# Optimization experiments

Hardware: AMD Instinct MI355X
Metric: run time of the kernel (lower is better)

The kernel has to match this reference:

```python
import jax, jax.numpy as jnp
import numpy as np

B, S, D, H = 2, 2048, 1024, 16
DK = D // H  # 64


def setup_inputs() -> dict:
    key = jax.random.key(0)
    ks = jax.random.split(key, 9)
    scale = 1.0 / np.sqrt(D)
    inp = {
        "q": jax.random.normal(ks[0], (B, S, D), dtype=jnp.float32),
        "k": jax.random.normal(ks[1], (B, S, D), dtype=jnp.float32),
        "v": jax.random.normal(ks[2], (B, S, D), dtype=jnp.float32),
        "Wq": jax.random.normal(ks[3], (D, D), dtype=jnp.float32) * scale,
        "bq": jax.random.normal(ks[4], (D,), dtype=jnp.float32) * scale,
        "Wk": jax.random.normal(ks[5], (D, D), dtype=jnp.float32) * scale,
        "bk": jax.random.normal(ks[6], (D,), dtype=jnp.float32) * scale,
        "Wv": jax.random.normal(ks[7], (D, D), dtype=jnp.float32) * scale,
        "bv": jax.random.normal(ks[8], (D,), dtype=jnp.float32) * scale,
        "mask": jnp.tril(jnp.ones((S, S), dtype=jnp.int32))[None, None],  # [1,1,S,S] causal
    }
    return inp


def reference(q, k, v, Wq, bq, Wk, bk, Wv, bv, mask):
    b, s, d = q.shape
    # QKV projections -> [B, H, S, DK]
    qh = (q @ Wq + bq).reshape(b, s, H, DK).transpose(0, 2, 1, 3)
    kh = (k @ Wk + bk).reshape(b, s, H, DK).transpose(0, 2, 1, 3)
    vh = (v @ Wv + bv).reshape(b, s, H, DK).transpose(0, 2, 1, 3)
    # scores [B, H, Sq, Sk]
    scores = jnp.einsum("bhqd,bhkd->bhqk", qh, kh) / jnp.sqrt(jnp.float32(DK))
    scores = jnp.where(mask == 0, jnp.float32(-1e9), scores)
    attn = jax.nn.softmax(scores, axis=-1)  # dropout is identity at inference
    out = jnp.einsum("bhqk,bhkd->bhqd", attn, vh)
    return out.transpose(0, 2, 1, 3).reshape(b, s, d)
```

## Files before the change

### kernel.cpp

```cpp
#include <hip/hip_runtime.h>
#include <hip/hip_bf16.h>

#define D_MODEL 1024
#define SEQ 2048
#define NH 16
#define DKH 64
#define MROWS 4096

typedef __attribute__((ext_vector_type(8))) short bf16x8;
typedef __attribute__((ext_vector_type(4))) float f32x4;
typedef __attribute__((ext_vector_type(4))) int int4v;

__device__ inline short f2bf(float f) {
    __hip_bfloat16 h = __float2bfloat16(f);
    return __builtin_bit_cast(short, h);
}

#define GLOAD16(gsrc, ldst)                                                     \
    __builtin_amdgcn_global_load_lds(                                           \
        (const __attribute__((address_space(1))) void*)(gsrc),                  \
        (__attribute__((address_space(3))) void*)(ldst), 16, 0, 0)

__global__ __launch_bounds__(256) void prep_kernel(
    const float* __restrict__ q, const float* __restrict__ k,
    const float* __restrict__ v,
    const float* __restrict__ Wq, const float* __restrict__ Wk,
    const float* __restrict__ Wv,
    short* __restrict__ aqkv, short* __restrict__ Wt) {
    __shared__ float tile[32][33];
    const int bx = blockIdx.x;
    if (bx < 6144) {
        const int z = bx >> 11;
        const int blk = bx & 2047;
        const float* src = (z == 0) ? q : (z == 1) ? k : v;
        short* dst = aqkv + (size_t)z * MROWS * D_MODEL;
        const size_t i = ((size_t)blk * 256 + threadIdx.x) * 8;
        float4 f0 = *(const float4*)(src + i);
        float4 f1 = *(const float4*)(src + i + 4);
        bf16x8 p;
        p[0] = f2bf(f0.x); p[1] = f2bf(f0.y); p[2] = f2bf(f0.z); p[3] = f2bf(f0.w);
        p[4] = f2bf(f1.x); p[5] = f2bf(f1.y); p[6] = f2bf(f1.z); p[7] = f2bf(f1.w);
        *(bf16x8*)(dst + i) = p;
    } else {
        int b = bx - 6144;
        const int z = b >> 10; b &= 1023;
        const float* W = (z == 0) ? Wq : (z == 1) ? Wk : Wv;
        short* dst = Wt + (size_t)z * D_MODEL * D_MODEL;
        const int n0 = (b & 31) * 32, k0 = (b >> 5) * 32;
        const int tx = threadIdx.x & 31, ty = threadIdx.x >> 5;
        for (int i = 0; i < 4; ++i)
            tile[ty + 8 * i][tx] = W[(size_t)(k0 + ty + 8 * i) * D_MODEL + n0 + tx];
        __syncthreads();
        for (int i = 0; i < 4; ++i)
            dst[(size_t)(n0 + ty + 8 * i) * D_MODEL + k0 + tx] = f2bf(tile[tx][ty + 8 * i]);
    }
}

__global__ __launch_bounds__(256) void proj_kernel(
    const short* __restrict__ aqkv, const short* __restrict__ Wt,
    const float* __restrict__ bq, const float* __restrict__ bk, const float* __restrict__ bv,
    short* __restrict__ qh, short* __restrict__ kh, short* __restrict__ vT) {
    __shared__ short sA[128 * 64];
    __shared__ short sB[128 * 64];

    const int z = blockIdx.z;
    const short* A = aqkv + (size_t)z * MROWS * D_MODEL;
    const short* B = Wt + (size_t)z * D_MODEL * D_MODEL;
    const float* bias = (z == 0) ? bq : (z == 1) ? bk : bv;
    short* dst = (z == 0) ? qh : (z == 1) ? kh : vT;

    const int m0 = blockIdx.y * 128;
    const int n0 = blockIdx.x * 128;
    const int tid = threadIdx.x;
    const int lane = tid & 63;
    const int w = tid >> 6;
    const int wr = w >> 1, wc = w & 1;
    const int lg = lane >> 4, ll = lane & 15;

    const int c0 = w * 4;
    const int srow = lane >> 3;
    const int scol = ((lane & 7) ^ srow) << 3;

    const int cs0 = ((lg * 16) ^ ((ll & 7) << 4)) >> 1;
    const int cs1 = ((64 + lg * 16) ^ ((ll & 7) << 4)) >> 1;

    f32x4 acc[4][4] = {};

    for (int kt = 0; kt < D_MODEL / 64; ++kt) {
        const int kk0 = kt * 64;
        __syncthreads();
        for (int i = 0; i < 4; ++i) {
            const int c = c0 + i;
            const int row = c * 8 + srow;
            GLOAD16(A + (size_t)(m0 + row) * D_MODEL + kk0 + scol, &sA[c * 512]);
            GLOAD16(B + (size_t)(n0 + row) * D_MODEL + kk0 + scol, &sB[c * 512]);
        }
        __syncthreads();

        bf16x8 af[4][2], bfr[4][2];
        for (int i = 0; i < 4; ++i) {
            const int rb = (wr * 64 + i * 16 + ll) * 64;
            af[i][0] = *(const bf16x8*)&sA[rb + cs0];
            af[i][1] = *(const bf16x8*)&sA[rb + cs1];
        }
        for (int j = 0; j < 4; ++j) {
            const int rb = (wc * 64 + j * 16 + ll) * 64;
            bfr[j][0] = *(const bf16x8*)&sB[rb + cs0];
            bfr[j][1] = *(const bf16x8*)&sB[rb + cs1];
        }
        for (int kk = 0; kk < 2; ++kk)
            for (int i = 0; i < 4; ++i)
                for (int j = 0; j < 4; ++j)
                    acc[i][j] = __builtin_amdgcn_mfma_f32_16x16x32_bf16(af[i][kk], bfr[j][kk], acc[i][j], 0, 0, 0);
    }

    for (int j = 0; j < 4; ++j) {
        const int n = n0 + wc * 64 + j * 16 + ll;
        const float bn = bias[n];
        const int h = n >> 6, dk = n & 63;
        for (int i = 0; i < 4; ++i) {
            for (int rr = 0; rr < 4; ++rr) {
                const int m = m0 + wr * 64 + i * 16 + lg * 4 + rr;
                float val = acc[i][j][rr] + bn;
                if (z == 0) val *= 0.125f;
                const int b = m >> 11, s = m & 2047;
                size_t idx;
                if (z < 2) idx = (((size_t)(b * NH + h)) * SEQ + s) * DKH + dk;
                else       idx = (((size_t)(b * NH + h)) * DKH + dk) * SEQ + s;
                dst[idx] = f2bf(val);
            }
        }
    }
}

__global__ __launch_bounds__(256) void attn_kernel(
    const short* __restrict__ qh, const short* __restrict__ kh,
    const short* __restrict__ vT, float* __restrict__ out) {
    __shared__ short sK[2][64 * 64];
    __shared__ short sV[2][64 * 64];
    __shared__ short sP[4][16 * 72];

    const int p = blockIdx.x;
    const int bh = blockIdx.y;
    const int tid = threadIdx.x;
    const int w = tid >> 6;
    const int lane = tid & 63;
    const int lg = lane >> 4, ll = lane & 15;
    const int b = bh >> 4, h = bh & 15;

    const short* kbase = kh + (size_t)bh * SEQ * DKH;
    const short* vbase = vT + (size_t)bh * DKH * SEQ;

    const int srow = lane >> 3;
    const int scol = ((lane & 7) ^ srow) << 3;
    const int cs0 = ((lg * 16) ^ ((ll & 7) << 4)) >> 1;
    const int cs1 = ((64 + lg * 16) ^ ((ll & 7) << 4)) >> 1;

#define ASTAGE(buf, t)                                                          \
    for (int c_ = 2 * w; c_ < 2 * w + 2; ++c_) {                                \
        const int row_ = c_ * 8 + srow;                                         \
        GLOAD16(kbase + (size_t)((t) * 64 + row_) * DKH + scol, &sK[buf][c_ * 512]); \
        GLOAD16(vbase + (size_t)row_ * SEQ + (t) * 64 + scol, &sV[buf][c_ * 512]);   \
    }

    for (int half = 0; half < 2; ++half) {
        const int qt = half ? (31 - p) : p;
        const int q0 = qt * 64;

        bf16x8 qf[2];
        {
            const short* src = qh + (((size_t)bh * SEQ) + q0 + w * 16 + ll) * DKH + lg * 8;
            qf[0] = *(const bf16x8*)(src);
            qf[1] = *(const bf16x8*)(src + 32);
        }

        f32x4 acc[4] = {};
        float m_i[4], l_i[4];
        for (int r = 0; r < 4; ++r) { m_i[r] = -1e30f; l_i[r] = 0.f; }

        const int ntiles = qt + 1;
        int cur = 0;
        ASTAGE(0, 0);
        __syncthreads();

        for (int t = 0; t < ntiles; ++t) {
            if (t + 1 < ntiles) ASTAGE(cur ^ 1, t + 1);

            f32x4 sc[4] = {};
            __builtin_amdgcn_s_setprio(1);
            for (int j = 0; j < 4; ++j) {
                const int rb = (j * 16 + ll) * 64;
                bf16x8 kf0 = *(const bf16x8*)&sK[cur][rb + cs0];
                bf16x8 kf1 = *(const bf16x8*)&sK[cur][rb + cs1];
                sc[j] = __builtin_amdgcn_mfma_f32_16x16x32_bf16(qf[0], kf0, sc[j], 0, 0, 0);
                sc[j] = __builtin_amdgcn_mfma_f32_16x16x32_bf16(qf[1], kf1, sc[j], 0, 0, 0);
            }
            __builtin_amdgcn_s_setprio(0);

            if (t == ntiles - 1) {
                const int k0 = t * 64;
                for (int j = 0; j < 4; ++j) {
                    const int key = k0 + j * 16 + ll;
                    for (int r = 0; r < 4; ++r) {
                        const int qrow = q0 + w * 16 + lg * 4 + r;
                        if (key > qrow) sc[j][r] = -1e30f;
                    }
                }
            }

            float tm[4];
            for (int r = 0; r < 4; ++r) {
                float t0 = fmaxf(fmaxf(sc[0][r], sc[1][r]), fmaxf(sc[2][r], sc[3][r]));
                t0 = fmaxf(t0, __shfl_xor(t0, 1));
                t0 = fmaxf(t0, __shfl_xor(t0, 2));
                t0 = fmaxf(t0, __shfl_xor(t0, 4));
                t0 = fmaxf(t0, __shfl_xor(t0, 8));
                tm[r] = t0;
            }
            bool grow = (tm[0] > m_i[0] + 8.f) | (tm[1] > m_i[1] + 8.f) |
                        (tm[2] > m_i[2] + 8.f) | (tm[3] > m_i[3] + 8.f);
            if (__any(grow)) {
                float scale[4];
                for (int r = 0; r < 4; ++r) {
                    const float mn = fmaxf(m_i[r], tm[r]);
                    scale[r] = __expf(m_i[r] - mn);
                    m_i[r] = mn;
                    l_i[r] *= scale[r];
                }
                for (int j = 0; j < 4; ++j)
                    for (int r = 0; r < 4; ++r)
                        acc[j][r] *= scale[r];
            }
            float tsum[4];
            for (int r = 0; r < 4; ++r) {
                float ts = 0.f;
                for (int j = 0; j < 4; ++j) {
                    const float pv = __expf(sc[j][r] - m_i[r]);
                    sc[j][r] = pv;
                    ts += pv;
                }
                ts += __shfl_xor(ts, 1);
                ts += __shfl_xor(ts, 2);
                ts += __shfl_xor(ts, 4);
                ts += __shfl_xor(ts, 8);
                tsum[r] = ts;
            }
            for (int r = 0; r < 4; ++r) l_i[r] += tsum[r];

            for (int j = 0; j < 4; ++j)
                for (int r = 0; r < 4; ++r)
                    sP[w][(lg * 4 + r) * 72 + j * 16 + ll] = f2bf(sc[j][r]);

            bf16x8 pf0 = *(const bf16x8*)&sP[w][ll * 72 + lg * 8];
            bf16x8 pf1 = *(const bf16x8*)&sP[w][ll * 72 + lg * 8 + 32];

            __builtin_amdgcn_s_setprio(1);
            for (int j = 0; j < 4; ++j) {
                const int rb = (j * 16 + ll) * 64;
                bf16x8 vf0 = *(const bf16x8*)&sV[cur][rb + cs0];
                bf16x8 vf1 = *(const bf16x8*)&sV[cur][rb + cs1];
                acc[j] = __builtin_amdgcn_mfma_f32_16x16x32_bf16(pf0, vf0, acc[j], 0, 0, 0);
                acc[j] = __builtin_amdgcn_mfma_f32_16x16x32_bf16(pf1, vf1, acc[j], 0, 0, 0);
            }
            __builtin_amdgcn_s_setprio(0);

            __syncthreads();
            cur ^= 1;
        }

        for (int j = 0; j < 4; ++j) {
            for (int r = 0; r < 4; ++r) {
                const int qrow = q0 + w * 16 + lg * 4 + r;
                out[((size_t)(b * SEQ + qrow)) * D_MODEL + h * DKH + j * 16 + ll] =
                    acc[j][r] / l_i[r];
            }
        }
    }
#undef ASTAGE
}

extern "C" void kernel_launch(void* const* d_in, const int* in_sizes, int n_in,
                              void* d_out, int out_size, void* d_ws, size_t ws_size,
                              hipStream_t stream) {
    const float* q  = (const float*)d_in[0];
    const float* k  = (const float*)d_in[1];
    const float* v  = (const float*)d_in[2];
    const float* Wq = (const float*)d_in[3];
    const float* bq = (const float*)d_in[4];
    const float* Wk = (const float*)d_in[5];
    const float* bk = (const float*)d_in[6];
    const float* Wv = (const float*)d_in[7];
    const float* bv = (const float*)d_in[8];
    float* out = (float*)d_out;

    short* aqkv = (short*)d_ws;
    short* Wt = aqkv + (size_t)3 * MROWS * D_MODEL;
    short* qh = Wt + (size_t)3 * D_MODEL * D_MODEL;
    short* kh = qh + (size_t)MROWS * D_MODEL;
    short* vT = kh + (size_t)MROWS * D_MODEL;

    hipLaunchKernelGGL(prep_kernel, dim3(9216), dim3(256), 0, stream,
                       q, k, v, Wq, Wk, Wv, aqkv, Wt);
    hipLaunchKernelGGL(proj_kernel, dim3(8, 32, 3), dim3(256), 0, stream,
                       aqkv, Wt, bq, bk, bv, qh, kh, vT);
    hipLaunchKernelGGL(attn_kernel, dim3(16, 32), dim3(256), 0, stream, qh, kh, vT, out);
}
```

Baseline: 249.0 us.

## Launch one block per query tile, heaviest first, and always rescale softmax

The attention kernel previously paired query tiles p and 31-p in one block to balance causal work over 512 blocks. It now launches 1024 blocks with one query tile each, ordered so the longest causal tiles are scheduled first, relying on the hardware scheduler for balance. The lazy online-softmax rescale (only when the max grew by more than 8, with a wave-wide vote) is replaced by an unconditional rescale every tile. This removes a branch and the vote, but adds exponentials and multiplies on every tile.

New measurement: 241.8 us. -2.9%, faster.

```diff
diff --git a/kernel.cpp b/kernel.cpp
--- a/kernel.cpp
+++ b/kernel.cpp
@@ -140,8 +140,10 @@
     __shared__ short sV[2][64 * 64];
     __shared__ short sP[4][16 * 72];
 
-    const int p = blockIdx.x;
-    const int bh = blockIdx.y;
+    const int flat = blockIdx.x;
+    const int qt = 31 - (flat >> 5);
+    const int bh = flat & 31;
+    const int q0 = qt * 64;
     const int tid = threadIdx.x;
     const int w = tid >> 6;
     const int lane = tid & 63;
@@ -163,117 +165,100 @@
         GLOAD16(vbase + (size_t)row_ * SEQ + (t) * 64 + scol, &sV[buf][c_ * 512]);   \
     }
 
-    for (int half = 0; half < 2; ++half) {
-        const int qt = half ? (31 - p) : p;
-        const int q0 = qt * 64;
-
-        bf16x8 qf[2];
-        {
-            const short* src = qh + (((size_t)bh * SEQ) + q0 + w * 16 + ll) * DKH + lg * 8;
-            qf[0] = *(const bf16x8*)(src);
-            qf[1] = *(const bf16x8*)(src + 32);
-        }
-
-        f32x4 acc[4] = {};
-        float m_i[4], l_i[4];
-        for (int r = 0; r < 4; ++r) { m_i[r] = -1e30f; l_i[r] = 0.f; }
-
-        const int ntiles = qt + 1;
-        int cur = 0;
-        ASTAGE(0, 0);
-        __syncthreads();
-
-        for (int t = 0; t < ntiles; ++t) {
-            if (t + 1 < ntiles) ASTAGE(cur ^ 1, t + 1);
-
-            f32x4 sc[4] = {};
-            __builtin_amdgcn_s_setprio(1);
+    bf16x8 qf[2];
+    {
+        const short* src = qh + (((size_t)bh * SEQ) + q0 + w * 16 + ll) * DKH + lg * 8;
+        qf[0] = *(const bf16x8*)(src);
+        qf[1] = *(const bf16x8*)(src + 32);
+    }
+
+    f32x4 acc[4] = {};
+    float m_i[4], l_i[4];
+    for (int r = 0; r < 4; ++r) { m_i[r] = -1e30f; l_i[r] = 0.f; }
+
+    const int ntiles = qt + 1;
+    int cur = 0;
+    ASTAGE(0, 0);
+    __syncthreads();
+
+    for (int t = 0; t < ntiles; ++t) {
+        if (t + 1 < ntiles) ASTAGE(cur ^ 1, t + 1);
+
+        f32x4 sc[4] = {};
+        __builtin_amdgcn_s_setprio(1);
+        for (int j = 0; j < 4; ++j) {
+            const int rb = (j * 16 + ll) * 64;
+            bf16x8 kf0 = *(const bf16x8*)&sK[cur][rb + cs0];
+            bf16x8 kf1 = *(const bf16x8*)&sK[cur][rb + cs1];
+            sc[j] = __builtin_amdgcn_mfma_f32_16x16x32_bf16(qf[0], kf0, sc[j], 0, 0, 0);
+            sc[j] = __builtin_amdgcn_mfma_f32_16x16x32_bf16(qf[1], kf1, sc[j], 0, 0, 0);
+        }
+        __builtin_amdgcn_s_setprio(0);
+
+        if (t == ntiles - 1) {
+            const int k0 = t * 64;
             for (int j = 0; j < 4; ++j) {
-                const int rb = (j * 16 + ll) * 64;
-                bf16x8 kf0 = *(const bf16x8*)&sK[cur][rb + cs0];
-                bf16x8 kf1 = *(const bf16x8*)&sK[cur][rb + cs1];
-                sc[j] = __builtin_amdgcn_mfma_f32_16x16x32_bf16(qf[0], kf0, sc[j], 0, 0, 0);
-                sc[j] = __builtin_amdgcn_mfma_f32_16x16x32_bf16(qf[1], kf1, sc[j], 0, 0, 0);
-            }
-            __builtin_amdgcn_s_setprio(0);
-
-            if (t == ntiles - 1) {
-                const int k0 = t * 64;
-                for (int j = 0; j < 4; ++j) {
-                    const int key = k0 + j * 16 + ll;
-                    for (int r = 0; r < 4; ++r) {
-                        const int qrow = q0 + w * 16 + lg * 4 + r;
-                        if (key > qrow) sc[j][r] = -1e30f;
-                    }
+                const int key = k0 + j * 16 + ll;
+                for (int r = 0; r < 4; ++r) {
+                    const int qrow = q0 + w * 16 + lg * 4 + r;
+                    if (key > qrow) sc[j][r] = -1e30f;
                 }
             }
-
-            float tm[4];
-            for (int r = 0; r < 4; ++r) {
-                float t0 = fmaxf(fmaxf(sc[0][r], sc[1][r]), fmaxf(sc[2][r], sc[3][r]));
-                t0 = fmaxf(t0, __shfl_xor(t0, 1));
-                t0 = fmaxf(t0, __shfl_xor(t0, 2));
-                t0 = fmaxf(t0, __shfl_xor(t0, 4));
-                t0 = fmaxf(t0, __shfl_xor(t0, 8));
-                tm[r] = t0;
+        }
+
+        float scale[4], tsum[4];
+        for (int r = 0; r < 4; ++r) {
+            float tm = fmaxf(fmaxf(sc[0][r], sc[1][r]), fmaxf(sc[2][r], sc[3][r]));
+            tm = fmaxf(tm, __shfl_xor(tm, 1));
+            tm = fmaxf(tm, __shfl_xor(tm, 2));
+            tm = fmaxf(tm, __shfl_xor(tm, 4));
+            tm = fmaxf(tm, __shfl_xor(tm, 8));
+            const float mn = fmaxf(m_i[r], tm);
+            scale[r] = __expf(m_i[r] - mn);
+            m_i[r] = mn;
+            float ts = 0.f;
+            for (int j = 0; j < 4; ++j) {
+                const float pv = __expf(sc[j][r] - mn);
+                sc[j][r] = pv;
+                ts += pv;
             }
-            bool grow = (tm[0] > m_i[0] + 8.f) | (tm[1] > m_i[1] + 8.f) |
-                        (tm[2] > m_i[2] + 8.f) | (tm[3] > m_i[3] + 8.f);
-            if (__any(grow)) {
-                float scale[4];
-                for (int r = 0; r < 4; ++r) {
-                    const float mn = fmaxf(m_i[r], tm[r]);
-                    scale[r] = __expf(m_i[r] - mn);
-                    m_i[r] = mn;
-                    l_i[r] *= scale[r];
-                }
-                for (int j = 0; j < 4; ++j)
-                    for (int r = 0; r < 4; ++r)
-                        acc[j][r] *= scale[r];
-            }
-            float tsum[4];
-            for (int r = 0; r < 4; ++r) {
-                float ts = 0.f;
-                for (int j = 0; j < 4; ++j) {
-                    const float pv = __expf(sc[j][r] - m_i[r]);
-                    sc[j][r] = pv;
-                    ts += pv;
-                }
-                ts += __shfl_xor(ts, 1);
-                ts += __shfl_xor(ts, 2);
-                ts += __shfl_xor(ts, 4);
-                ts += __shfl_xor(ts, 8);
-                tsum[r] = ts;
-            }
-            for (int r = 0; r < 4; ++r) l_i[r] += tsum[r];
-
-            for (int j = 0; j < 4; ++j)
-                for (int r = 0; r < 4; ++r)
-                    sP[w][(lg * 4 + r) * 72 + j * 16 + ll] = f2bf(sc[j][r]);
-
-            bf16x8 pf0 = *(const bf16x8*)&sP[w][ll * 72 + lg * 8];
-            bf16x8 pf1 = *(const bf16x8*)&sP[w][ll * 72 + lg * 8 + 32];
-
-            __builtin_amdgcn_s_setprio(1);
-            for (int j = 0; j < 4; ++j) {
-                const int rb = (j * 16 + ll) * 64;
-                bf16x8 vf0 = *(const bf16x8*)&sV[cur][rb + cs0];
-                bf16x8 vf1 = *(const bf16x8*)&sV[cur][rb + cs1];
-                acc[j] = __builtin_amdgcn_mfma_f32_16x16x32_bf16(pf0, vf0, acc[j], 0, 0, 0);
-                acc[j] = __builtin_amdgcn_mfma_f32_16x16x32_bf16(pf1, vf1, acc[j], 0, 0, 0);
-            }
-            __builtin_amdgcn_s_setprio(0);
-
-            __syncthreads();
-            cur ^= 1;
-        }
-
+            ts += __shfl_xor(ts, 1);
+            ts += __shfl_xor(ts, 2);
+            ts += __shfl_xor(ts, 4);
+            ts += __shfl_xor(ts, 8);
+            tsum[r] = ts;
+        }
+        for (int r = 0; r < 4; ++r) l_i[r] = l_i[r] * scale[r] + tsum[r];
+        for (int j = 0; j < 4; ++j)
+            for (int r = 0; r < 4; ++r)
+                acc[j][r] *= scale[r];
+
+        for (int j = 0; j < 4; ++j)
+            for (int r = 0; r < 4; ++r)
+                sP[w][(lg * 4 + r) * 72 + j * 16 + ll] = f2bf(sc[j][r]);
+
+        bf16x8 pf0 = *(const bf16x8*)&sP[w][ll * 72 + lg * 8];
+        bf16x8 pf1 = *(const bf16x8*)&sP[w][ll * 72 + lg * 8 + 32];
+
+        __builtin_amdgcn_s_setprio(1);
         for (int j = 0; j < 4; ++j) {
-            for (int r = 0; r < 4; ++r) {
-                const int qrow = q0 + w * 16 + lg * 4 + r;
-                out[((size_t)(b * SEQ + qrow)) * D_MODEL + h * DKH + j * 16 + ll] =
-                    acc[j][r] / l_i[r];
-            }
+            const int rb = (j * 16 + ll) * 64;
+            bf16x8 vf0 = *(const bf16x8*)&sV[cur][rb + cs0];
+            bf16x8 vf1 = *(const bf16x8*)&sV[cur][rb + cs1];
+            acc[j] = __builtin_amdgcn_mfma_f32_16x16x32_bf16(pf0, vf0, acc[j], 0, 0, 0);
+            acc[j] = __builtin_amdgcn_mfma_f32_16x16x32_bf16(pf1, vf1, acc[j], 0, 0, 0);
+        }
+        __builtin_amdgcn_s_setprio(0);
+
+        __syncthreads();
+        cur ^= 1;
+    }
+
+    for (int j = 0; j < 4; ++j) {
+        for (int r = 0; r < 4; ++r) {
+            const int qrow = q0 + w * 16 + lg * 4 + r;
+            out[((size_t)(b * SEQ + qrow)) * D_MODEL + h * DKH + j * 16 + ll] =
+                acc[j][r] / l_i[r];
         }
     }
 #undef ASTAGE
@@ -303,5 +288,5 @@
                        q, k, v, Wq, Wk, Wv, aqkv, Wt);
     hipLaunchKernelGGL(proj_kernel, dim3(8, 32, 3), dim3(256), 0, stream,
                        aqkv, Wt, bq, bk, bv, qh, kh, vT);
-    hipLaunchKernelGGL(attn_kernel, dim3(16, 32), dim3(256), 0, stream, qh, kh, vT, out);
-}
+    hipLaunchKernelGGL(attn_kernel, dim3(1024), dim3(256), 0, stream, qh, kh, vT, out);
+}
```
